# Kernel optimization log

Hardware: AMD Instinct MI355X
Metric: run time of the kernel (lower is better)

The kernel has to match this reference:

```python
import jax, jax.numpy as jnp
import numpy as np

N, E, G = 2048, 65536, 32
F_ATOM, LAT, IN, ED, NB, L = 16, 64, 128, 32, 5, 5


def setup_inputs() -> dict:
    key = jax.random.key(0)
    ks = iter(jax.random.split(key, 64))
    nxt = lambda: next(ks)
    def w(shape):
        fan_in = shape[-2] if len(shape) >= 2 else 1
        return jax.random.normal(nxt(), shape, jnp.float32) / np.sqrt(fan_in)
    inp = {}
    inp['x'] = jax.random.normal(nxt(), (N, F_ATOM), jnp.float32)
    inp['t'] = jax.random.uniform(nxt(), (G, 1), jnp.float32)
    inp['z'] = jax.random.normal(nxt(), (N, LAT), jnp.float32)
    inp['edge_index'] = jax.random.randint(nxt(), (2, E), 0, N, jnp.int32)
    inp['edge_attr'] = jax.random.normal(nxt(), (E, NB), jnp.float32)
    inp['batch'] = jnp.sort(jax.random.randint(nxt(), (N,), 0, G, jnp.int32))
    inp['batch_edge_global'] = jax.random.randint(nxt(), (E,), 0, G, jnp.int32)
    # top-level dense layers
    inp['Wt_a'] = w((1, IN)); inp['bt_a'] = jnp.zeros((IN,))
    inp['Wt_b'] = w((1, ED)); inp['bt_b'] = jnp.zeros((ED,))
    inp['W_atom'] = w((F_ATOM, IN)); inp['b_atom'] = jnp.zeros((IN,))
    inp['W_bond'] = w((NB, ED)); inp['b_bond'] = jnp.zeros((ED,))
    inp['W_lat'] = w((LAT, IN)); inp['b_lat'] = jnp.zeros((IN,))
    inp['W_at'] = w((IN, IN)); inp['b_at'] = jnp.zeros((IN,))
    inp['W_bt'] = w((ED, ED)); inp['b_bt'] = jnp.zeros((ED,))
    # TopoEdgeGNN: L layers of edge-conditioned message passing with edge update
    inp['Wmsg'] = w((L, 2 * IN + ED, IN)); inp['bmsg'] = jnp.zeros((L, IN))
    inp['Wnode'] = w((L, 2 * IN, IN)); inp['bnode'] = jnp.zeros((L, IN))
    inp['Wedge'] = w((L, 2 * IN + ED, ED)); inp['bedge'] = jnp.zeros((L, ED))
    # prediction head
    inp['Wsh'] = w((IN, IN)); inp['bsh'] = jnp.zeros((IN,))
    inp['Wbm'] = w((ED, IN)); inp['bbm'] = jnp.zeros((IN,))
    inp['Wbl'] = w((IN, NB)); inp['bbl'] = jnp.zeros((NB,))
    inp['Wal'] = w((IN, F_ATOM + LAT)); inp['bal'] = jnp.zeros((F_ATOM + LAT,))
    return inp


def reference(x, t, z, edge_index, edge_attr, batch, batch_edge_global,
              Wt_a, bt_a, Wt_b, bt_b, W_atom, b_atom, W_bond, b_bond,
              W_lat, b_lat, W_at, b_at, W_bt, b_bt,
              Wmsg, bmsg, Wnode, bnode, Wedge, bedge,
              Wsh, bsh, Wbm, bbm, Wbl, bbl, Wal, bal):
    j, i = edge_index[0], edge_index[1]
    # time embeddings, gathered to nodes / edges
    ta = t @ Wt_a + bt_a            # [G, IN]
    tb = t @ Wt_b + bt_b            # [G, ED]
    tnode = ta[batch]               # [N, IN]
    tedge = tb[batch_edge_global]   # [E, ED]
    # node features
    s = x @ W_atom + b_atom
    s = (s + tnode) @ W_at + b_at
    s = s + (z @ W_lat + b_lat)
    # edge features
    e = edge_attr @ W_bond + b_bond
    e = (e + tedge) @ W_bt + b_bt
    # TopoEdgeGNN: message passing with residual node/edge updates
    for l in range(L):
        m = jax.nn.silu(jnp.concatenate([s[i], s[j], e], -1) @ Wmsg[l] + bmsg[l])  # [E, IN]
        agg = jax.ops.segment_sum(m, i, num_segments=N)                            # [N, IN]
        s = s + jax.nn.silu(jnp.concatenate([s, agg], -1) @ Wnode[l] + bnode[l])
        e = e + jax.nn.silu(jnp.concatenate([s[i], s[j], e], -1) @ Wedge[l] + bedge[l])
    # prediction head
    s2 = jax.nn.silu(s @ Wsh + bsh)
    al = s2 @ Wal + bal
    atoms_pred, latent_pred = al[:, :F_ATOM], al[:, F_ATOM:]
    # dense edge symmetrization: scatter edges into [N, N, ED], symmetrize, gather back
    e_dense = jnp.zeros((N, N, ED), e.dtype).at[j, i].set(e)
    e_dense = 0.5 * (e_dense + e_dense.transpose(1, 0, 2))
    e_sym = e_dense[j, i]           # [E, ED]
    f = jax.nn.silu(s2[i] + s2[j] + (e_sym @ Wbm + bbm))
    bonds_pred = f @ Wbl + bbl
    return latent_pred, atoms_pred, bonds_pred
```

## Files before the change

kernel.cpp:

```cpp
#include <hip/hip_runtime.h>
#include <hip/hip_bf16.h>

#define NN 2048
#define NE 65536
#define NG 32
#define CIN 128
#define CED 32
#define CLAT 64
#define CFA 16
#define CNB 5
#define NL 5

#define OFF_AT (NN * CLAT)
#define OFF_B  (NN * CLAT + NN * CFA)

typedef __attribute__((ext_vector_type(8))) short bf16x8;
typedef __attribute__((ext_vector_type(4))) float f32x4;

__device__ __forceinline__ float silu_f(float v) { return v / (1.0f + __expf(-v)); }
__device__ __forceinline__ short f2bs(float v) {
    __hip_bfloat16 h = __float2bfloat16(v);
    return *reinterpret_cast<short*>(&h);
}
__device__ __forceinline__ float bs2f(short s) {
    return __bfloat162float(*reinterpret_cast<__hip_bfloat16*>(&s));
}
__device__ __forceinline__ unsigned pack2(float a, float b) {
    return ((unsigned)(unsigned short)f2bs(b) << 16) | (unsigned short)f2bs(a);
}

struct KArgs {
    const float *x, *t, *z;
    const int *jj, *ii;
    const float *ea;
    const int *batch, *beg;
    const float *Wt_a, *bt_a, *Wt_b, *bt_b, *W_atom, *b_atom, *W_bond, *b_bond;
    const float *W_lat, *b_lat, *W_at, *b_at, *W_bt, *b_bt;
    const float *Wmsg, *bmsg, *Wnode, *bnode, *Wedge, *bedge;
    const float *Wsh, *bsh, *Wbm, *bbm, *Wbl, *bbl, *Wal, *bal;
    float *s, *e;
    float *agg;
    int *cnt, *rowpos, *rowstart, *invp, *i_s, *j_s;
    float *s2, *U, *V, *P, *Q;
    int *map;
    short *Wpn, *Wpsh, *Wpal, *Wpbm, *Wproj, *W3m, *We3;
    int *gsync;
    float *out;
};

__device__ __forceinline__ void gbar(int* gs)
{
    __syncthreads();
    if (threadIdx.x == 0) {
        __threadfence();
        int g = __hip_atomic_load(gs + 32, __ATOMIC_RELAXED, __HIP_MEMORY_SCOPE_AGENT);
        int* gc = gs + 64 + ((blockIdx.x >> 5) << 5);
        if (__hip_atomic_fetch_add(gc, 1, __ATOMIC_ACQ_REL, __HIP_MEMORY_SCOPE_AGENT) == 31) {
            __hip_atomic_store(gc, 0, __ATOMIC_RELAXED, __HIP_MEMORY_SCOPE_AGENT);
            if (__hip_atomic_fetch_add(gs, 1, __ATOMIC_ACQ_REL, __HIP_MEMORY_SCOPE_AGENT) == 31) {
                __hip_atomic_store(gs, 0, __ATOMIC_RELAXED, __HIP_MEMORY_SCOPE_AGENT);
                __hip_atomic_store(gs + 32, g + 1, __ATOMIC_RELEASE, __HIP_MEMORY_SCOPE_AGENT);
            }
        }
        while (__hip_atomic_load(gs + 32, __ATOMIC_RELAXED, __HIP_MEMORY_SCOPE_AGENT) == g)
            __builtin_amdgcn_s_sleep(8);
    }
    __syncthreads();
    __threadfence();
}

__device__ __forceinline__ void phase_pack(const KArgs& a, int start, int stride)
{
    for (int idx = start; idx < 6 * 4 * 20 * 64 * 8; idx += stride) {
        int j = idx & 7, t0 = idx >> 3, lane = t0 & 63, tt = t0 >> 6;
        int kq = (lane >> 4) * 8 + j, n16 = lane & 15;
        if (idx < NL * 8 * 8 * 64 * 8) {
            int nt = tt & 7, kt = (tt >> 3) & 7, l = tt >> 6;
            a.Wpn[idx] = f2bs(a.Wnode[((size_t)l * 256 + kt * 32 + kq) * CIN + nt * 16 + n16]);
        }
        if (idx < 4 * 8 * 64 * 8) {
            int nt = tt & 7, kt = tt >> 3;
            a.Wpsh[idx] = f2bs(a.Wsh[(size_t)(kt * 32 + kq) * CIN + nt * 16 + n16]);
        }
        if (idx < 4 * 5 * 64 * 8) {
            int nt = tt % 5, kt = tt / 5;
            a.Wpal[idx] = f2bs(a.Wal[(size_t)(kt * 32 + kq) * 80 + nt * 16 + n16]);
        }
        if (idx < 8 * 64 * 8) {
            int nt = tt & 7;
            a.Wpbm[idx] = f2bs(a.Wbm[(size_t)kq * CIN + nt * 16 + n16]);
        }
        {
            int nt = tt % 20; int t2 = tt / 20; int kt = t2 & 3; int slot = t2 >> 2;
            int k = kt * 32 + kq;
            float v;
            if (nt < 16) {
                int msgl = slot % 5;
                int srcK = (nt < 8) ? k : 128 + k;
                int col = (nt & 7) * 16 + n16;
                v = a.Wmsg[((size_t)msgl * 288 + srcK) * CIN + col];
            } else {
                int edgel = (slot == 0) ? 0 : slot - 1;
                int srcK = (nt < 18) ? k : 128 + k;
                int col = (nt & 1) * 16 + n16;
                v = a.Wedge[((size_t)edgel * 288 + srcK) * CED + col];
            }
            a.Wproj[idx] = f2bs(v);
        }
        if (idx < NL * 8 * 64 * 8) {
            int nt = tt & 7, l = tt >> 3;
            a.W3m[idx] = f2bs(a.Wmsg[((size_t)l * 288 + 256 + kq) * CIN + nt * 16 + n16]);
        }
        if (idx < NL * 2 * 64 * 8) {
            int nt = tt & 1, l = tt >> 1;
            a.We3[idx] = f2bs(a.Wedge[((size_t)l * 288 + 256 + kq) * CED + nt * 16 + n16]);
        }
    }
}

__device__ __forceinline__ void phase_init_s(const KArgs& a, char* smem, int tile, int tid)
{
    float* xs  = (float*)smem;
    float* zs  = (float*)(smem + 1024);
    float* tmp = (float*)(smem + 5120);
    float* tv  = (float*)(smem + 13312);
    int nb0 = tile * 16;
    int c = tid & 127, h = tid >> 7;
    if (tid < 16 * CFA / 4) ((float4*)xs)[tid] = ((const float4*)a.x)[nb0 * (CFA / 4) + tid];
    if (tid < 16 * CLAT / 4) ((float4*)zs)[tid] = ((const float4*)a.z)[nb0 * (CLAT / 4) + tid];
    if (tid < 16) tv[tid] = a.t[a.batch[nb0 + tid]];
    __syncthreads();
    float wta = a.Wt_a[c], base0 = a.b_atom[c] + a.bt_a[c];
    float acc[8];
#pragma unroll
    for (int q = 0; q < 8; q++) acc[q] = base0 + tv[h * 8 + q] * wta;
    for (int k = 0; k < CFA; k++) {
        float w = a.W_atom[k * CIN + c];
#pragma unroll
        for (int q = 0; q < 8; q++) acc[q] += xs[(h * 8 + q) * CFA + k] * w;
    }
#pragma unroll
    for (int q = 0; q < 8; q++) tmp[(h * 8 + q) * CIN + c] = acc[q];
    __syncthreads();
    float base1 = a.b_at[c] + a.b_lat[c];
    float acc2[8];
#pragma unroll
    for (int q = 0; q < 8; q++) acc2[q] = base1;
    for (int k4 = 0; k4 < CIN / 4; k4++) {
        float w0 = a.W_at[(4 * k4 + 0) * CIN + c], w1 = a.W_at[(4 * k4 + 1) * CIN + c];
        float w2 = a.W_at[(4 * k4 + 2) * CIN + c], w3 = a.W_at[(4 * k4 + 3) * CIN + c];
#pragma unroll
        for (int q = 0; q < 8; q++) {
            float4 f = *(const float4*)&tmp[(h * 8 + q) * CIN + 4 * k4];
            acc2[q] += f.x * w0 + f.y * w1 + f.z * w2 + f.w * w3;
        }
    }
    for (int k4 = 0; k4 < CLAT / 4; k4++) {
        float w0 = a.W_lat[(4 * k4 + 0) * CIN + c], w1 = a.W_lat[(4 * k4 + 1) * CIN + c];
        float w2 = a.W_lat[(4 * k4 + 2) * CIN + c], w3 = a.W_lat[(4 * k4 + 3) * CIN + c];
#pragma unroll
        for (int q = 0; q < 8; q++) {
            float4 f = *(const float4*)&zs[(h * 8 + q) * CLAT + 4 * k4];
            acc2[q] += f.x * w0 + f.y * w1 + f.z * w2 + f.w * w3;
        }
    }
#pragma unroll
    for (int q = 0; q < 8; q++) {
        int nd = nb0 + h * 8 + q;
        a.s[(size_t)nd * CIN + c] = acc2[q];
    }
}

__device__ __forceinline__ void phase_init_e(const KArgs& a, char* smem, int tb, int tid)
{
    float* eas   = (float*)smem;
    float* tv    = (float*)(smem + 1280);
    int*   sp    = (int*)(smem + 1536);
    float* tmp   = (float*)(smem + 1792);
    float* wbt   = (float*)(smem + 10240);
    float* wbond = (float*)(smem + 14336);
    float* cb    = (float*)(smem + 14976);
    float* wtb   = (float*)(smem + 15104);
    float* bbt2  = (float*)(smem + 15232);
    int k0 = tb * 64;
    for (int idx = tid; idx < 320; idx += 256) eas[idx] = a.ea[(size_t)k0 * 5 + idx];
    if (tid < 64) { tv[tid] = a.t[a.beg[k0 + tid]]; sp[tid] = a.invp[k0 + tid]; }
    for (int idx = tid; idx < 1024; idx += 256) wbt[idx] = a.W_bt[idx];
    if (tid < 160) wbond[tid] = a.W_bond[tid];
    if (tid < 32) { cb[tid] = a.b_bond[tid] + a.bt_b[tid]; wtb[tid] = a.Wt_b[tid]; bbt2[tid] = a.b_bt[tid]; }
    __syncthreads();
    int ch = tid & 31, eg = tid >> 5;
#pragma unroll
    for (int q = 0; q < 8; q++) {
        int le = eg * 8 + q;
        float acc = cb[ch] + tv[le] * wtb[ch];
#pragma unroll
        for (int bb = 0; bb < CNB; bb++) acc += eas[le * 5 + bb] * wbond[bb * 32 + ch];
        tmp[le * 33 + ch] = acc;
    }
    __syncthreads();
#pragma unroll
    for (int q = 0; q < 8; q++) {
        int le = eg * 8 + q;
        float acc2 = bbt2[ch];
        for (int d = 0; d < 32; d++) acc2 += tmp[le * 33 + d] * wbt[d * 32 + ch];
        size_t ix = (size_t)sp[le] * CED + ch;
        a.e[ix] = acc2;
        if (ch == 0) {
            int k = k0 + le;
            atomicMax(&a.map[(size_t)a.jj[k] * NN + a.ii[k]], k);
        }
    }
}

__device__ __forceinline__ void phase_node2(
    const KArgs& a, char* smem, int tile, int tid, bool DO_NODE, bool DO_POST,
    bool LOAD_S, bool STORE_S,
    const short* Wpn_l, const float* bnode_l, const short* Wproj_slot, float (*s_reg)[4])
{
    short* feat  = (short*)smem;
    short* feat2 = (short*)(smem + 8448);
    int nb0 = tile * 16;
    int lane = tid & 63, w = tid >> 6;
    int quad = lane >> 4, n16 = lane & 15;

    if (DO_NODE) {
#pragma unroll
        for (int n2 = 0; n2 < 2; n2++) {
            int col = (w * 2 + n2) * 16 + n16;
#pragma unroll
            for (int r = 0; r < 4; r++) {
                int row = quad * 4 + r;
                if (LOAD_S) s_reg[n2][r] = a.s[(size_t)(nb0 + row) * CIN + col];
                feat[row * 264 + col] = f2bs(s_reg[n2][r]);
            }
        }
#pragma unroll
        for (int k2 = 0; k2 < 2; k2++) {
            int idx = tid + k2 * 256;
            int kl = idx >> 5, c = idx & 31;
            size_t base = (size_t)(nb0 + kl) * 128 + c;
            float4 p0 = ((const float4*)a.agg)[base];
            float4 p1 = ((const float4*)a.agg)[base + 32];
            float4 p2 = ((const float4*)a.agg)[base + 64];
            float4 p3 = ((const float4*)a.agg)[base + 96];
            float4 z4 = {0.f, 0.f, 0.f, 0.f};
            ((float4*)a.agg)[base] = z4;
            ((float4*)a.agg)[base + 32] = z4;
            ((float4*)a.agg)[base + 64] = z4;
            ((float4*)a.agg)[base + 96] = z4;
            float4 v; v.x = p0.x + p1.x + p2.x + p3.x; v.y = p0.y + p1.y + p2.y + p3.y;
            v.z = p0.z + p1.z + p2.z + p3.z; v.w = p0.w + p1.w + p2.w + p3.w;
            uint2 p; p.x = pack2(v.x, v.y); p.y = pack2(v.z, v.w);
            *(uint2*)&feat[kl * 264 + 128 + 4 * c] = p;
        }
        __syncthreads();
        f32x4 acc[2];
        acc[0] = (f32x4){0.f, 0.f, 0.f, 0.f};
        acc[1] = (f32x4){0.f, 0.f, 0.f, 0.f};
        const short* fbase = feat + n16 * 264 + quad * 8;
#pragma unroll
        for (int kt = 0; kt < 8; kt++) {
            bf16x8 av = *(const bf16x8*)(fbase + kt * 32);
#pragma unroll
            for (int n2 = 0; n2 < 2; n2++) {
                int nt = w * 2 + n2;
                bf16x8 b = *(const bf16x8*)(Wpn_l + ((size_t)(kt * 8 + nt) * 64 + lane) * 8);
                acc[n2] = __builtin_amdgcn_mfma_f32_16x16x32_bf16(av, b, acc[n2], 0, 0, 0);
            }
        }
#pragma unroll
        for (int n2 = 0; n2 < 2; n2++) {
            int col = (w * 2 + n2) * 16 + n16;
            float bb = bnode_l[col];
#pragma unroll
            for (int r = 0; r < 4; r++) {
                int row = quad * 4 + r;
                float v = s_reg[n2][r] + silu_f(acc[n2][r] + bb);
                s_reg[n2][r] = v;
                if (STORE_S) a.s[(size_t)(nb0 + row) * CIN + col] = v;
                feat2[row * 136 + col] = f2bs(v);
            }
        }
        __syncthreads();
    } else {
        int kl = tid >> 4, c = tid & 15;
        const float4* sp4 = (const float4*)&a.s[(size_t)(nb0 + kl) * CIN + c * 8];
        float4 v0 = sp4[0], v1 = sp4[1];
        uint4 p; p.x = pack2(v0.x, v0.y); p.y = pack2(v0.z, v0.w);
        p.z = pack2(v1.x, v1.y); p.w = pack2(v1.z, v1.w);
        *(uint4*)&feat2[kl * 136 + c * 8] = p;
        __syncthreads();
    }

    {
        f32x4 accp[5];
#pragma unroll
        for (int t2 = 0; t2 < 5; t2++) accp[t2] = (f32x4){0.f, 0.f, 0.f, 0.f};
        const short* abase = feat2 + n16 * 136 + quad * 8;
#pragma unroll
        for (int kt = 0; kt < 4; kt++) {
            bf16x8 av = *(const bf16x8*)(abase + kt * 32);
#pragma unroll
            for (int n5 = 0; n5 < 5; n5++) {
                int nt = w * 5 + n5;
                bf16x8 b = *(const bf16x8*)(Wproj_slot + ((size_t)(kt * 20 + nt) * 64 + lane) * 8);
                accp[n5] = __builtin_amdgcn_mfma_f32_16x16x32_bf16(av, b, accp[n5], 0, 0, 0);
            }
        }
#pragma unroll
        for (int n5 = 0; n5 < 5; n5++) {
            int nt = w * 5 + n5;
#pragma unroll
            for (int r = 0; r < 4; r++) {
                int node = tile * 16 + quad * 4 + r;
                float v = accp[n5][r];
                if (nt < 8)       a.U[(size_t)node * CIN + nt * 16 + n16] = v;
                else if (nt < 16) a.V[(size_t)node * CIN + (nt - 8) * 16 + n16] = v;
                else if (nt < 18) a.P[(size_t)node * CED + (nt - 16) * 16 + n16] = v;
                else              a.Q[(size_t)node * CED + (nt - 18) * 16 + n16] = v;
            }
        }
    }

    if (DO_POST) {
        short* feat_s2 = feat;
        const short* fbase = feat2 + n16 * 136 + quad * 8;
        f32x4 acc[2];
        acc[0] = (f32x4){0.f, 0.f, 0.f, 0.f};
        acc[1] = (f32x4){0.f, 0.f, 0.f, 0.f};
#pragma unroll
        for (int kt = 0; kt < 4; kt++) {
            bf16x8 av = *(const bf16x8*)(fbase + kt * 32);
#pragma unroll
            for (int n2 = 0; n2 < 2; n2++) {
                int nt = w * 2 + n2;
                bf16x8 b = *(const bf16x8*)(a.Wpsh + ((size_t)(kt * 8 + nt) * 64 + lane) * 8);
                acc[n2] = __builtin_amdgcn_mfma_f32_16x16x32_bf16(av, b, acc[n2], 0, 0, 0);
            }
        }
#pragma unroll
        for (int n2 = 0; n2 < 2; n2++) {
            int col = (w * 2 + n2) * 16 + n16;
            float bb = a.bsh[col];
#pragma unroll
            for (int r = 0; r < 4; r++) {
                int row = quad * 4 + r;
                float v = silu_f(acc[n2][r] + bb);
                a.s2[(size_t)(nb0 + row) * CIN + col] = v;
                feat_s2[row * 136 + col] = f2bs(v);
            }
        }
        __syncthreads();
        const short* abase2 = feat_s2 + n16 * 136 + quad * 8;
        f32x4 acca[2];
        acca[0] = (f32x4){0.f, 0.f, 0.f, 0.f};
        acca[1] = (f32x4){0.f, 0.f, 0.f, 0.f};
        int nAl = (w == 0) ? 2 : 1;
        int ntl[2] = {w, 4};
#pragma unroll
        for (int kt = 0; kt < 4; kt++) {
            bf16x8 av = *(const bf16x8*)(abase2 + kt * 32);
#pragma unroll
            for (int q = 0; q < 2; q++) {
                if (q < nAl) {
                    bf16x8 b = *(const bf16x8*)(a.Wpal + ((size_t)(kt * 5 + ntl[q]) * 64 + lane) * 8);
                    acca[q] = __builtin_amdgcn_mfma_f32_16x16x32_bf16(av, b, acca[q], 0, 0, 0);
                }
            }
        }
#pragma unroll
        for (int q = 0; q < 2; q++) {
            if (q < nAl) {
                int col = ntl[q] * 16 + n16;
                float bb = a.bal[col];
#pragma unroll
                for (int r = 0; r < 4; r++) {
                    int node = nb0 + quad * 4 + r;
                    float v = acca[q][r] + bb;
                    if (col < CFA) a.out[OFF_AT + node * CFA + col] = v;
                    else           a.out[(size_t)node * CLAT + (col - CFA)] = v;
                }
            }
        }
    }
}

__device__ __forceinline__ void phase_em2(
    const KArgs& a, char* smem, int tb, int tid, bool DO_EDGE, bool DO_MSG, bool LOAD_E, bool WRITE_E,
    const short* We3p, const float* bedge_l, const short* W3mp, const float* bmsg_l,
    float (*e_reg)[4])
{
    short* feat_e = (short*)smem;
    short* uv_bf  = (short*)(smem + 5120);
    short* pq_bf  = (short*)(smem + 22528);
    int*   sii    = (int*)(smem + 27648);
    int*   sjj    = (int*)(smem + 27904);
    int e0 = tb * 64;
    int lane = tid & 63, w = tid >> 6;
    int quad = lane >> 4, n16 = lane & 15;
    if (tid < 64) sii[tid] = a.i_s[e0 + tid];
    else if (tid < 128) sjj[tid - 64] = a.j_s[e0 + tid - 64];
    __syncthreads();
#pragma unroll
    for (int nt = 0; nt < 2; nt++) {
        int ch = nt * 16 + n16;
#pragma unroll
        for (int r = 0; r < 4; r++) {
            int el = w * 16 + quad * 4 + r;
            if (LOAD_E) e_reg[nt][r] = a.e[(size_t)(e0 + el) * CED + ch];
            feat_e[el * 40 + ch] = f2bs(e_reg[nt][r]);
        }
    }
    if (DO_EDGE) {
        float4 pa[2], qb[2];
#pragma unroll
        for (int k2 = 0; k2 < 2; k2++) {
            int idx = tid + k2 * 256;
            int kl = idx >> 3, c = idx & 7;
            pa[k2] = ((const float4*)a.P)[(size_t)sii[kl] * 8 + c];
            qb[k2] = ((const float4*)a.Q)[(size_t)sjj[kl] * 8 + c];
        }
#pragma unroll
        for (int k2 = 0; k2 < 2; k2++) {
            int idx = tid + k2 * 256;
            int kl = idx >> 3, c = idx & 7;
            uint2 p; p.x = pack2(pa[k2].x + qb[k2].x, pa[k2].y + qb[k2].y);
            p.y = pack2(pa[k2].z + qb[k2].z, pa[k2].w + qb[k2].w);
            *(uint2*)&pq_bf[kl * 40 + 4 * c] = p;
        }
    }
    if (DO_MSG) {
#pragma unroll
        for (int half = 0; half < 2; half++) {
            float4 avv[4], bvv[4];
#pragma unroll
            for (int k2 = 0; k2 < 4; k2++) {
                int idx = tid + (half * 4 + k2) * 256;
                int kl = idx >> 5, c = idx & 31;
                avv[k2] = ((const float4*)a.U)[(size_t)sii[kl] * 32 + c];
                bvv[k2] = ((const float4*)a.V)[(size_t)sjj[kl] * 32 + c];
            }
#pragma unroll
            for (int k2 = 0; k2 < 4; k2++) {
                int idx = tid + (half * 4 + k2) * 256;
                int kl = idx >> 5, c = idx & 31;
                uint2 p; p.x = pack2(avv[k2].x + bvv[k2].x, avv[k2].y + bvv[k2].y);
                p.y = pack2(avv[k2].z + bvv[k2].z, avv[k2].w + bvv[k2].w);
                *(uint2*)&uv_bf[kl * 136 + 4 * c] = p;
            }
        }
    }
    __syncthreads();
    const short* abase = feat_e + (w * 16 + n16) * 40 + quad * 8;
    bf16x8 av = *(const bf16x8*)abase;

    if (DO_EDGE) {
        f32x4 acc_e[2];
        acc_e[0] = (f32x4){0.f, 0.f, 0.f, 0.f};
        acc_e[1] = (f32x4){0.f, 0.f, 0.f, 0.f};
#pragma unroll
        for (int nt = 0; nt < 2; nt++) {
            bf16x8 b = *(const bf16x8*)(We3p + ((size_t)(nt * 64 + lane)) * 8);
            acc_e[nt] = __builtin_amdgcn_mfma_f32_16x16x32_bf16(av, b, acc_e[nt], 0, 0, 0);
        }
#pragma unroll
        for (int nt = 0; nt < 2; nt++) {
            int ch = nt * 16 + n16;
            float bb = bedge_l[ch];
#pragma unroll
            for (int r = 0; r < 4; r++) {
                int el = w * 16 + quad * 4 + r;
                float v = e_reg[nt][r] + silu_f(acc_e[nt][r] + bb + bs2f(pq_bf[el * 40 + ch]));
                e_reg[nt][r] = v;
                feat_e[el * 40 + ch] = f2bs(v);
                if (WRITE_E) a.e[(size_t)(e0 + el) * CED + ch] = v;
            }
        }
        av = *(const bf16x8*)abase;
    }

    if (DO_MSG) {
        f32x4 acc_m[8];
#pragma unroll
        for (int t2 = 0; t2 < 8; t2++) acc_m[t2] = (f32x4){0.f, 0.f, 0.f, 0.f};
#pragma unroll
        for (int nt = 0; nt < 8; nt++) {
            bf16x8 b = *(const bf16x8*)(W3mp + ((size_t)(nt * 64 + lane)) * 8);
            acc_m[nt] = __builtin_amdgcn_mfma_f32_16x16x32_bf16(av, b, acc_m[nt], 0, 0, 0);
        }
#pragma unroll
        for (int nt = 0; nt < 8; nt++) {
            int ch = nt * 16 + n16;
            float bb = bmsg_l[ch];
#pragma unroll
            for (int r = 0; r < 4; r++) {
                int el = w * 16 + quad * 4 + r;
                int lix = el * 136 + ch;
                float m = silu_f(acc_m[nt][r] + bb + bs2f(uv_bf[lix]));
                uv_bf[lix] = f2bs(m);
            }
        }
        __syncthreads();
        if (tid < 128) {
            int c = tid;
            float run = 0.f;
            int cur = sii[0];
            for (int r = 0; r < 64; r++) {
                int tg = sii[r];
                if (tg != cur) {
                    int slot = tb - (a.rowstart[cur] >> 6); slot = (slot > 3) ? 3 : slot;
                    a.agg[((size_t)cur * 4 + slot) * CIN + c] = run;
                    run = 0.f; cur = tg;
                }
                run += bs2f(uv_bf[r * 136 + c]);
            }
            int slot = tb - (a.rowstart[cur] >> 6); slot = (slot > 3) ? 3 : slot;
            a.agg[((size_t)cur * 4 + slot) * CIN + c] = run;
        }
    }
}

__device__ __forceinline__ void phase_post_edge(const KArgs& a, char* smem, int tb, int tid)
{
    short* esym  = (short*)smem;
    short* sbias = (short*)(smem + 5120);
    int* sii = (int*)(smem + 22016);
    int* sjj = (int*)(smem + 22272);
    int* skf = (int*)(smem + 22528);
    int* skb = (int*)(smem + 22784);
    int e0 = tb * 64;
    if (tid < 64) sii[tid] = a.ii[e0 + tid];
    else if (tid < 128) sjj[tid - 64] = a.jj[e0 + tid - 64];
    __syncthreads();
    if (tid < 64) skf[tid] = a.invp[a.map[(size_t)sjj[tid] * NN + sii[tid]]];
    else if (tid < 128) {
        int m = a.map[(size_t)sii[tid - 64] * NN + sjj[tid - 64]];
        skb[tid - 64] = (m >= 0) ? a.invp[m] : -1;
    }
    __syncthreads();
    {
        float4 av2[2], bv2[2];
#pragma unroll
        for (int k2 = 0; k2 < 2; k2++) {
            int idx = tid + k2 * 256;
            int kl = idx >> 3, c = idx & 7;
            av2[k2] = ((const float4*)a.e)[(size_t)skf[kl] * 8 + c];
            int kb = skb[kl];
            bv2[k2] = (float4){0.f, 0.f, 0.f, 0.f};
            if (kb >= 0) bv2[k2] = ((const float4*)a.e)[(size_t)kb * 8 + c];
        }
#pragma unroll
        for (int k2 = 0; k2 < 2; k2++) {
            int idx = tid + k2 * 256;
            int kl = idx >> 3, c = idx & 7;
            uint2 p; p.x = pack2(0.5f * (av2[k2].x + bv2[k2].x), 0.5f * (av2[k2].y + bv2[k2].y));
            p.y = pack2(0.5f * (av2[k2].z + bv2[k2].z), 0.5f * (av2[k2].w + bv2[k2].w));
            *(uint2*)&esym[kl * 40 + 4 * c] = p;
        }
    }
#pragma unroll
    for (int half = 0; half < 2; half++) {
        float4 av4[4], bv4[4];
#pragma unroll
        for (int k2 = 0; k2 < 4; k2++) {
            int idx = tid + (half * 4 + k2) * 256;
            int kl = idx >> 5, c = idx & 31;
            av4[k2] = ((const float4*)a.s2)[(size_t)sii[kl] * 32 + c];
            bv4[k2] = ((const float4*)a.s2)[(size_t)sjj[kl] * 32 + c];
        }
#pragma unroll
        for (int k2 = 0; k2 < 4; k2++) {
            int idx = tid + (half * 4 + k2) * 256;
            int kl = idx >> 5, c = idx & 31;
            uint2 p; p.x = pack2(av4[k2].x + bv4[k2].x, av4[k2].y + bv4[k2].y);
            p.y = pack2(av4[k2].z + bv4[k2].z, av4[k2].w + bv4[k2].w);
            *(uint2*)&sbias[kl * 132 + 4 * c] = p;
        }
    }
    __syncthreads();
    int lane = tid & 63, w = tid >> 6;
    int quad = lane >> 4, n16 = lane & 15;
    bf16x8 av = *(const bf16x8*)(esym + (w * 16 + n16) * 40 + quad * 8);
    f32x4 acc[8];
#pragma unroll
    for (int nt = 0; nt < 8; nt++) {
        bf16x8 b = *(const bf16x8*)(a.Wpbm + ((size_t)nt * 64 + lane) * 8);
        f32x4 zero = {0.f, 0.f, 0.f, 0.f};
        acc[nt] = __builtin_amdgcn_mfma_f32_16x16x32_bf16(av, b, zero, 0, 0, 0);
    }
    float f[8][4];
#pragma unroll
    for (int nt = 0; nt < 8; nt++) {
        int col = nt * 16 + n16;
        float bb = a.bbm[col];
#pragma unroll
        for (int r = 0; r < 4; r++) {
            int row = w * 16 + quad * 4 + r;
            f[nt][r] = silu_f(acc[nt][r] + bb + bs2f(sbias[row * 132 + col]));
        }
    }
    __syncthreads();
    short* fshT = sbias;
#pragma unroll
    for (int nt = 0; nt < 8; nt++) {
        int col = nt * 16 + n16;
#pragma unroll
        for (int r = 0; r < 4; r++) {
            int row = w * 16 + quad * 4 + r;
            fshT[col * 66 + row] = f2bs(f[nt][r]);
        }
    }
    __syncthreads();
    for (int idx = tid; idx < 64 * CNB; idx += 256) {
        int kl = idx / CNB, b = idx - kl * CNB;
        float acc3 = a.bbl[b];
        for (int d = 0; d < CIN; d++) acc3 += bs2f(fshT[d * 66 + kl]) * a.Wbl[d * CNB + b];
        a.out[OFF_B + (size_t)(e0 + kl) * CNB + b] = acc3;
    }
}

__global__ __launch_bounds__(256, 4) void k_main(KArgs a)
{
    __shared__ __align__(16) char smem[28160];
    int bid = blockIdx.x, tid = threadIdx.x;
    int* gs = a.gsync;
    float s_reg[2][4], e_reg[2][4];

    {
        float4 z4 = {0.f, 0.f, 0.f, 0.f};
        ((float4*)a.agg)[bid * 256 + tid] = z4;
    }
    if (bid < 128) phase_init_s(a, smem, bid, tid);
    else phase_pack(a, (bid - 128) * 256 + tid, 896 * 256);
    if (bid >= 192 && bid < 448) atomicAdd(&a.cnt[a.ii[(bid - 192) * 256 + tid]], 1);
    {
        int4 m1 = {-1, -1, -1, -1};
#pragma unroll
        for (int q = 0; q < 4; q++)
            ((int4*)a.map)[(size_t)bid * 1024 + q * 256 + tid] = m1;
    }
    gbar(gs);

    if (bid == 0) {
        int* part = (int*)smem;
        int loc[8], sum = 0;
#pragma unroll
        for (int q = 0; q < 8; q++) { loc[q] = a.cnt[tid * 8 + q]; sum += loc[q]; }
        part[tid] = sum;
        __syncthreads();
        if (tid == 0) { int r = 0; for (int i = 0; i < 256; i++) { int v = part[i]; part[i] = r; r += v; } }
        __syncthreads();
        int r = part[tid];
#pragma unroll
        for (int q = 0; q < 8; q++) { a.rowpos[tid * 8 + q] = r; a.rowstart[tid * 8 + q] = r; r += loc[q]; }
        __syncthreads();
    }
    if (bid < 128) phase_node2(a, smem, bid, tid, false, false, false, false,
                               nullptr, nullptr, a.Wproj, s_reg);
    gbar(gs);

    if (bid < 256) {
        int k = bid * 256 + tid;
        int iv = a.ii[k];
        int p = atomicAdd(&a.rowpos[iv], 1);
        a.invp[k] = p;
        a.i_s[p] = iv;
        a.j_s[p] = a.jj[k];
    }
    gbar(gs);

    phase_init_e(a, smem, bid, tid);
    gbar(gs);

    phase_em2(a, smem, bid, tid, false, true, true, false, nullptr, nullptr, a.W3m, a.bmsg, e_reg);
    gbar(gs);

    for (int l = 0; l < NL; l++) {
        if (bid < 128)
            phase_node2(a, smem, bid, tid, true, l == NL - 1, l == 0, false,
                        a.Wpn + (size_t)l * 8 * 8 * 64 * 8, a.bnode + l * CIN,
                        a.Wproj + (size_t)(l + 1) * 4 * 20 * 64 * 8, s_reg);
        gbar(gs);
        bool dm = (l < NL - 1);
        phase_em2(a, smem, bid, tid, true, dm, false, l == NL - 1,
                  a.We3 + (size_t)l * 2 * 64 * 8, a.bedge + l * CED,
                  dm ? a.W3m + (size_t)(l + 1) * 8 * 64 * 8 : a.W3m,
                  dm ? a.bmsg + (l + 1) * CIN : a.bmsg, e_reg);
        gbar(gs);
    }

    phase_post_edge(a, smem, bid, tid);
}

__global__ __launch_bounds__(256) void k_prologue(KArgs a)
{
    __shared__ __align__(16) char smem[13440];
    int b = blockIdx.x, tid = threadIdx.x;
    if (b < 960) phase_pack(a, b * 256 + tid, 960 * 256);
    else if (b < 1088) phase_init_s(a, smem, b - 960, tid);
    else {
        int base = (b - 1088) * 1024;
#pragma unroll
        for (int q = 0; q < 4; q++) atomicAdd(&a.cnt[a.ii[base + q * 256 + tid]], 1);
    }
}
__global__ __launch_bounds__(256) void k_prefix(KArgs a)
{
    __shared__ int part[256];
    int tid = threadIdx.x;
    int loc[8], sum = 0;
#pragma unroll
    for (int q = 0; q < 8; q++) { loc[q] = a.cnt[tid * 8 + q]; sum += loc[q]; }
    part[tid] = sum;
    __syncthreads();
    if (tid == 0) { int r = 0; for (int i = 0; i < 256; i++) { int v = part[i]; part[i] = r; r += v; } }
    __syncthreads();
    int r = part[tid];
#pragma unroll
    for (int q = 0; q < 8; q++) { a.rowpos[tid * 8 + q] = r; a.rowstart[tid * 8 + q] = r; r += loc[q]; }
}
__global__ void k_perm(KArgs a)
{
    int k = blockIdx.x * 256 + threadIdx.x;
    int iv = a.ii[k];
    int p = atomicAdd(&a.rowpos[iv], 1);
    a.invp[k] = p;
    a.i_s[p] = iv;
    a.j_s[p] = a.jj[k];
}
__global__ __launch_bounds__(256) void k_init_e(KArgs a)
{
    __shared__ __align__(16) char smem[15360];
    phase_init_e(a, smem, blockIdx.x, threadIdx.x);
}
__global__ __launch_bounds__(256) void k_node_proj(KArgs a, int donode, int dopost,
                                                   const short* Wpn_l, const float* bnode_l,
                                                   const short* Wproj_slot)
{
    __shared__ __align__(16) char smem[12800];
    float s_reg[2][4];
    phase_node2(a, smem, blockIdx.x, threadIdx.x, donode != 0, dopost != 0,
                donode != 0, donode != 0, Wpn_l, bnode_l, Wproj_slot, s_reg);
}
__global__ __launch_bounds__(256) void k_em(KArgs a, int de, int dm, const short* We3p,
                                            const float* bedge_l, const short* W3mp, const float* bmsg_l)
{
    __shared__ __align__(16) char smem[28160];
    float e_reg[2][4];
    phase_em2(a, smem, blockIdx.x, threadIdx.x, de != 0, dm != 0, true, de != 0,
              We3p, bedge_l, W3mp, bmsg_l, e_reg);
}
__global__ __launch_bounds__(256) void k_post_edge(KArgs a)
{
    __shared__ __align__(16) char smem[23040];
    phase_post_edge(a, smem, blockIdx.x, threadIdx.x);
}

extern "C" void kernel_launch(void* const* d_in, const int* in_sizes, int n_in,
                              void* d_out, int out_size, void* d_ws, size_t ws_size,
                              hipStream_t stream) {
    KArgs a;
    a.x      = (const float*)d_in[0];
    a.t      = (const float*)d_in[1];
    a.z      = (const float*)d_in[2];
    const int* eidx = (const int*)d_in[3];
    a.jj     = eidx;
    a.ii     = eidx + NE;
    a.ea     = (const float*)d_in[4];
    a.batch  = (const int*)d_in[5];
    a.beg    = (const int*)d_in[6];
    a.Wt_a   = (const float*)d_in[7];
    a.bt_a   = (const float*)d_in[8];
    a.Wt_b   = (const float*)d_in[9];
    a.bt_b   = (const float*)d_in[10];
    a.W_atom = (const float*)d_in[11];
    a.b_atom = (const float*)d_in[12];
    a.W_bond = (const float*)d_in[13];
    a.b_bond = (const float*)d_in[14];
    a.W_lat  = (const float*)d_in[15];
    a.b_lat  = (const float*)d_in[16];
    a.W_at   = (const float*)d_in[17];
    a.b_at   = (const float*)d_in[18];
    a.W_bt   = (const float*)d_in[19];
    a.b_bt   = (const float*)d_in[20];
    a.Wmsg   = (const float*)d_in[21];
    a.bmsg   = (const float*)d_in[22];
    a.Wnode  = (const float*)d_in[23];
    a.bnode  = (const float*)d_in[24];
    a.Wedge  = (const float*)d_in[25];
    a.bedge  = (const float*)d_in[26];
    a.Wsh    = (const float*)d_in[27];
    a.bsh    = (const float*)d_in[28];
    a.Wbm    = (const float*)d_in[29];
    a.bbm    = (const float*)d_in[30];
    a.Wbl    = (const float*)d_in[31];
    a.bbl    = (const float*)d_in[32];
    a.Wal    = (const float*)d_in[33];
    a.bal    = (const float*)d_in[34];

    a.s        = (float*)d_ws;
    a.e        = a.s + (size_t)NN * CIN;
    a.agg      = a.e + (size_t)NE * CED;
    a.cnt      = (int*)(a.agg + (size_t)NN * 4 * CIN);
    a.rowpos   = a.cnt + NN;
    a.rowstart = a.rowpos + NN;
    a.invp     = a.rowstart + NN;
    a.i_s      = a.invp + NE;
    a.j_s      = a.i_s + NE;
    a.s2       = (float*)(a.j_s + NE);
    a.U        = a.s2 + (size_t)NN * CIN;
    a.V        = a.U + (size_t)NN * CIN;
    a.P        = a.V + (size_t)NN * CIN;
    a.Q        = a.P + (size_t)NN * CED;
    a.map      = (int*)(a.Q + (size_t)NN * CED);
    a.Wpn      = (short*)(a.map + (size_t)NN * NN);
    a.Wpsh     = a.Wpn + (size_t)NL * 8 * 8 * 64 * 8;
    a.Wpal     = a.Wpsh + (size_t)4 * 8 * 64 * 8;
    a.Wpbm     = a.Wpal + (size_t)4 * 5 * 64 * 8;
    a.Wproj    = a.Wpbm + (size_t)8 * 64 * 8;
    a.W3m      = a.Wproj + (size_t)6 * 4 * 20 * 64 * 8;
    a.We3      = a.W3m + (size_t)NL * 8 * 64 * 8;
    a.gsync    = (int*)(a.We3 + (size_t)NL * 2 * 64 * 8);
    a.out      = (float*)d_out;

    static int use_fused = -1;
    if (use_fused < 0) {
        int dev = 0;
        (void)hipGetDevice(&dev);
        hipDeviceProp_t props;
        int ncu = 0;
        if (hipGetDeviceProperties(&props, dev) == hipSuccess) ncu = props.multiProcessorCount;
        int maxb = 0;
        if (hipOccupancyMaxActiveBlocksPerMultiprocessor(&maxb, k_main, 256, 0) != hipSuccess) maxb = 0;
        use_fused = ((long)maxb * ncu >= 1024) ? 1 : 0;
    }

    if (use_fused) {
        hipMemsetAsync(a.gsync, 0, (64 + 32 * 32) * sizeof(int), stream);
        hipMemsetAsync(a.cnt, 0, NN * sizeof(int), stream);
        k_main<<<1024, 256, 0, stream>>>(a);
    } else {
        hipMemsetAsync(a.map, 0xFF, (size_t)NN * NN * sizeof(int), stream);
        hipMemsetAsync(a.agg, 0, ((size_t)NN * 4 * CIN) * sizeof(float) + NN * sizeof(int), stream);
        k_prologue<<<1152, 256, 0, stream>>>(a);
        k_prefix<<<1, 256, 0, stream>>>(a);
        k_perm<<<NE / 256, 256, 0, stream>>>(a);
        k_init_e<<<NE / 64, 256, 0, stream>>>(a);
        k_node_proj<<<NN / 16, 256, 0, stream>>>(a, 0, 0, nullptr, nullptr, a.Wproj);
        k_em<<<NE / 64, 256, 0, stream>>>(a, 0, 1, nullptr, nullptr, a.W3m, a.bmsg);
        for (int l = 0; l < NL; l++) {
            int dopost = (l == NL - 1) ? 1 : 0;
            k_node_proj<<<NN / 16, 256, 0, stream>>>(a, 1, dopost,
                a.Wpn + (size_t)l * 8 * 8 * 64 * 8, a.bnode + l * CIN,
                a.Wproj + (size_t)(l + 1) * 4 * 20 * 64 * 8);
            int dm = (l < NL - 1) ? 1 : 0;
            k_em<<<NE / 64, 256, 0, stream>>>(a, 1, dm,
                a.We3 + (size_t)l * 2 * 64 * 8, a.bedge + l * CED,
                dm ? a.W3m + (size_t)(l + 1) * 8 * 64 * 8 : a.W3m,
                dm ? a.bmsg + (l + 1) * CIN : a.bmsg);
        }
        k_post_edge<<<NE / 64, 256, 0, stream>>>(a);
    }
}
```

Baseline: 354.4 us.

## Store node projections and s2 in bf16 and force multi-kernel path

Stores the per-node projection buffers U, V, P, Q and the head activation s2 as bf16 instead of fp32. This halves the bytes moved by the per-edge gathers, and the gathered pairs are added after converting back to float. It also hardcodes the non-fused multi-kernel path in place of the occupancy-based choice of the cooperative fused kernel. The cost is extra rounding before the add, and the fused path can no longer be selected.

```diff
diff --git a/kernel.cpp b/kernel.cpp
--- a/kernel.cpp
+++ b/kernel.cpp
@@ -27,6 +27,11 @@
 }
 __device__ __forceinline__ unsigned pack2(float a, float b) {
     return ((unsigned)(unsigned short)f2bs(b) << 16) | (unsigned short)f2bs(a);
+}
+__device__ __forceinline__ unsigned addpack(unsigned ua, unsigned va) {
+    float a0 = bs2f((short)(ua & 0xffff)), a1 = bs2f((short)(ua >> 16));
+    float b0 = bs2f((short)(va & 0xffff)), b1 = bs2f((short)(va >> 16));
+    return pack2(a0 + b0, a1 + b1);
 }
 
 struct KArgs {
@@ -41,7 +46,7 @@
     float *s, *e;
     float *agg;
     int *cnt, *rowpos, *rowstart, *invp, *i_s, *j_s;
-    float *s2, *U, *V, *P, *Q;
+    short *s2, *U, *V, *P, *Q;
     int *map;
     short *Wpn, *Wpsh, *Wpal, *Wpbm, *Wproj, *W3m, *We3;
     int *gsync;
@@ -314,11 +319,11 @@
 #pragma unroll
             for (int r = 0; r < 4; r++) {
                 int node = tile * 16 + quad * 4 + r;
-                float v = accp[n5][r];
-                if (nt < 8)       a.U[(size_t)node * CIN + nt * 16 + n16] = v;
-                else if (nt < 16) a.V[(size_t)node * CIN + (nt - 8) * 16 + n16] = v;
-                else if (nt < 18) a.P[(size_t)node * CED + (nt - 16) * 16 + n16] = v;
-                else              a.Q[(size_t)node * CED + (nt - 18) * 16 + n16] = v;
+                short bv = f2bs(accp[n5][r]);
+                if (nt < 8)       a.U[(size_t)node * CIN + nt * 16 + n16] = bv;
+                else if (nt < 16) a.V[(size_t)node * CIN + (nt - 8) * 16 + n16] = bv;
+                else if (nt < 18) a.P[(size_t)node * CED + (nt - 16) * 16 + n16] = bv;
+                else              a.Q[(size_t)node * CED + (nt - 18) * 16 + n16] = bv;
             }
         }
     }
@@ -347,8 +352,9 @@
             for (int r = 0; r < 4; r++) {
                 int row = quad * 4 + r;
                 float v = silu_f(acc[n2][r] + bb);
-                a.s2[(size_t)(nb0 + row) * CIN + col] = v;
-                feat_s2[row * 136 + col] = f2bs(v);
+                short bv = f2bs(v);
+                a.s2[(size_t)(nb0 + row) * CIN + col] = bv;
+                feat_s2[row * 136 + col] = bv;
             }
         }
         __syncthreads();
@@ -413,42 +419,38 @@
         }
     }
     if (DO_EDGE) {
-        float4 pa[2], qb[2];
+        uint2 pa[2], qb[2];
 #pragma unroll
         for (int k2 = 0; k2 < 2; k2++) {
             int idx = tid + k2 * 256;
             int kl = idx >> 3, c = idx & 7;
-            pa[k2] = ((const float4*)a.P)[(size_t)sii[kl] * 8 + c];
-            qb[k2] = ((const float4*)a.Q)[(size_t)sjj[kl] * 8 + c];
+            pa[k2] = ((const uint2*)a.P)[(size_t)sii[kl] * 8 + c];
+            qb[k2] = ((const uint2*)a.Q)[(size_t)sjj[kl] * 8 + c];
         }
 #pragma unroll
         for (int k2 = 0; k2 < 2; k2++) {
             int idx = tid + k2 * 256;
             int kl = idx >> 3, c = idx & 7;
-            uint2 p; p.x = pack2(pa[k2].x + qb[k2].x, pa[k2].y + qb[k2].y);
-            p.y = pack2(pa[k2].z + qb[k2].z, pa[k2].w + qb[k2].w);
-            *(uint2*)&pq_bf[kl * 40 + 4 * c] = p;
+            uint2 o; o.x = addpack(pa[k2].x, qb[k2].x); o.y = addpack(pa[k2].y, qb[k2].y);
+            *(uint2*)&pq_bf[kl * 40 + 4 * c] = o;
         }
     }
     if (DO_MSG) {
-#pragma unroll
-        for (int half = 0; half < 2; half++) {
-            float4 avv[4], bvv[4];
-#pragma unroll
-            for (int k2 = 0; k2 < 4; k2++) {
-                int idx = tid + (half * 4 + k2) * 256;
-                int kl = idx >> 5, c = idx & 31;
-                avv[k2] = ((const float4*)a.U)[(size_t)sii[kl] * 32 + c];
-                bvv[k2] = ((const float4*)a.V)[(size_t)sjj[kl] * 32 + c];
-            }
-#pragma unroll
-            for (int k2 = 0; k2 < 4; k2++) {
-                int idx = tid + (half * 4 + k2) * 256;
-                int kl = idx >> 5, c = idx & 31;
-                uint2 p; p.x = pack2(avv[k2].x + bvv[k2].x, avv[k2].y + bvv[k2].y);
-                p.y = pack2(avv[k2].z + bvv[k2].z, avv[k2].w + bvv[k2].w);
-                *(uint2*)&uv_bf[kl * 136 + 4 * c] = p;
-            }
+        uint4 ua[4], va[4];
+#pragma unroll
+        for (int k2 = 0; k2 < 4; k2++) {
+            int idx = tid + k2 * 256;
+            int kl = idx >> 4, c = idx & 15;
+            ua[k2] = ((const uint4*)a.U)[(size_t)sii[kl] * 16 + c];
+            va[k2] = ((const uint4*)a.V)[(size_t)sjj[kl] * 16 + c];
+        }
+#pragma unroll
+        for (int k2 = 0; k2 < 4; k2++) {
+            int idx = tid + k2 * 256;
+            int kl = idx >> 4, c = idx & 15;
+            uint4 o; o.x = addpack(ua[k2].x, va[k2].x); o.y = addpack(ua[k2].y, va[k2].y);
+            o.z = addpack(ua[k2].z, va[k2].z); o.w = addpack(ua[k2].w, va[k2].w);
+            *(uint4*)&uv_bf[kl * 136 + c * 8] = o;
         }
     }
     __syncthreads();
@@ -561,21 +563,20 @@
     }
 #pragma unroll
     for (int half = 0; half < 2; half++) {
-        float4 av4[4], bv4[4];
+        uint2 av4[4], bv4[4];
 #pragma unroll
         for (int k2 = 0; k2 < 4; k2++) {
             int idx = tid + (half * 4 + k2) * 256;
             int kl = idx >> 5, c = idx & 31;
-            av4[k2] = ((const float4*)a.s2)[(size_t)sii[kl] * 32 + c];
-            bv4[k2] = ((const float4*)a.s2)[(size_t)sjj[kl] * 32 + c];
+            av4[k2] = ((const uint2*)a.s2)[(size_t)sii[kl] * 32 + c];
+            bv4[k2] = ((const uint2*)a.s2)[(size_t)sjj[kl] * 32 + c];
         }
 #pragma unroll
         for (int k2 = 0; k2 < 4; k2++) {
             int idx = tid + (half * 4 + k2) * 256;
             int kl = idx >> 5, c = idx & 31;
-            uint2 p; p.x = pack2(av4[k2].x + bv4[k2].x, av4[k2].y + bv4[k2].y);
-            p.y = pack2(av4[k2].z + bv4[k2].z, av4[k2].w + bv4[k2].w);
-            *(uint2*)&sbias[kl * 132 + 4 * c] = p;
+            uint2 o; o.x = addpack(av4[k2].x, bv4[k2].x); o.y = addpack(av4[k2].y, bv4[k2].y);
+            *(uint2*)&sbias[kl * 132 + 4 * c] = o;
         }
     }
     __syncthreads();
@@ -808,7 +809,7 @@
     a.invp     = a.rowstart + NN;
     a.i_s      = a.invp + NE;
     a.j_s      = a.i_s + NE;
-    a.s2       = (float*)(a.j_s + NE);
+    a.s2       = (short*)(a.j_s + NE);
     a.U        = a.s2 + (size_t)NN * CIN;
     a.V        = a.U + (size_t)NN * CIN;
     a.P        = a.V + (size_t)NN * CIN;
@@ -824,17 +825,7 @@
     a.gsync    = (int*)(a.We3 + (size_t)NL * 2 * 64 * 8);
     a.out      = (float*)d_out;
 
-    static int use_fused = -1;
-    if (use_fused < 0) {
-        int dev = 0;
-        (void)hipGetDevice(&dev);
-        hipDeviceProp_t props;
-        int ncu = 0;
-        if (hipGetDeviceProperties(&props, dev) == hipSuccess) ncu = props.multiProcessorCount;
-        int maxb = 0;
-        if (hipOccupancyMaxActiveBlocksPerMultiprocessor(&maxb, k_main, 256, 0) != hipSuccess) maxb = 0;
-        use_fused = ((long)maxb * ncu >= 1024) ? 1 : 0;
-    }
+    int use_fused = 0;
 
     if (use_fused) {
         hipMemsetAsync(a.gsync, 0, (64 + 32 * 32) * sizeof(int), stream);
@@ -842,7 +833,7 @@
         k_main<<<1024, 256, 0, stream>>>(a);
     } else {
         hipMemsetAsync(a.map, 0xFF, (size_t)NN * NN * sizeof(int), stream);
-        hipMemsetAsync(a.agg, 0, ((size_t)NN * 4 * CIN) * sizeof(float) + NN * sizeof(int), stream);
+        hipMemsetAsync(a.agg, 0, (size_t)NN * 4 * CIN * sizeof(float) + NN * sizeof(int), stream);
         k_prologue<<<1152, 256, 0, stream>>>(a);
         k_prefix<<<1, 256, 0, stream>>>(a);
         k_perm<<<NE / 256, 256, 0, stream>>>(a);
```

Result: faster. 340.6 us (-3.9%).
